# Performance work log

Measured on AMD Instinct MI355X. Metric: run time of the kernel, lower is better.

The kernel has to match this reference:

```python
import jax, jax.numpy as jnp
import numpy as np

V, T, NS, NH, E, H = 4, 4, 100000, 12288, 100000, 64
NEG_SLOPE = 0.01  # nn.LeakyReLU default


def setup_inputs() -> dict:
    key = jax.random.key(0)
    k1, k2, k3, k4, k5 = jax.random.split(key, 5)
    x = jax.random.normal(k1, (V, T, NS), dtype=jnp.float32)          # per-var, per-t scalar node features
    src_idx = jax.random.randint(k2, (V, T, E), 0, NS, dtype=jnp.int32)
    dst_idx = jax.random.randint(k3, (V, T, E), 0, NH, dtype=jnp.int32)
    W = jax.random.normal(k4, (V, T, H), dtype=jnp.float32)            # GraphConv weight, in_feats=1 -> [1,H] per etype
    b = jax.random.normal(k5, (V, T, H), dtype=jnp.float32) * 0.02     # GraphConv bias per etype
    return {"x": x, "W": W, "b": b, "src_idx": src_idx, "dst_idx": dst_idx, "n_healpix": NH}


def reference(x, W, b, src_idx, dst_idx, n_healpix):
    # x: [V,T,NS]; W,b: [V,T,H]; src_idx,dst_idx: [V,T,E]
    x = jnp.nan_to_num(x, nan=0.0)

    def conv_scalar(x_v, src, dst):
        # x_v: [T,NS] (all timestep features for this var), src/dst: [E] for ONE edge type
        ones = jnp.ones(src.shape, x_v.dtype)
        deg_out = jax.ops.segment_sum(ones, src, num_segments=NS)       # out-degree of src nodes
        deg_in = jax.ops.segment_sum(ones, dst, num_segments=n_healpix)  # in-degree of dst nodes
        norm_src = jax.lax.rsqrt(jnp.maximum(deg_out, 1.0))
        norm_dst = jax.lax.rsqrt(jnp.maximum(deg_in, 1.0))
        msg = x_v[:, src] * norm_src[src]                                # [T,E] gather
        agg = jax.vmap(lambda m: jax.ops.segment_sum(m, dst, num_segments=n_healpix))(msg)  # [T,NH]
        return agg * norm_dst                                            # norm='both'

    # HeteroGraphConv bug-faithful: for each var, EVERY per-t' conv is applied to each x[:,t]
    # s[v, t', t, n] = normalized scatter of x[v,t] through edges of etype t'
    s = jax.vmap(lambda xv, sv, dv: jax.vmap(lambda se, de: conv_scalar(xv, se, de))(sv, dv))(
        x, src_idx, dst_idx)                                             # [V,T',T,NH]

    # in_feats=1: linear is outer product with W row; bias + LeakyReLU inside each conv, sum over etypes t'
    h = jax.nn.leaky_relu(s[..., None] * W[:, :, None, None, :] + b[:, :, None, None, :],
                          negative_slope=NEG_SLOPE)                      # [V,T',T,NH,H]
    out = h.sum(axis=1)                                                  # aggregate='sum' over edge types -> [V,T,NH,H]
    # final stacking: stack over t (dim=1) then over vars (dim=1) -> [NH, V, T, H]
    return jnp.transpose(out, (2, 0, 1, 3))
```

## Files before the change

### kernel.cpp

```cpp
#include <hip/hip_runtime.h>
#include <math.h>

#define V    4
#define T    4
#define NSRC 100000
#define NHX  12288
#define E    100000
#define H    64
#define VT   16

#define SL    16
#define SLE   (E/SL)
#define RCH   2
#define RBINS (NSRC/RCH)
#define RW    (RBINS/4)
#define HF    8
#define HE    (E/HF)
#define NW    (NSRC/4)
#define NCH   12
#define NPB   8

#define S1_TRANS  391
#define S1_CNT    (RCH*HF*VT)
#define S1_DHIST  (SL*VT)
#define S2_SCAN   (NCH*VT)
#define S2_NSFIN  391

typedef float vf4 __attribute__((ext_vector_type(4)));

__global__ void __launch_bounds__(1024)
s1_kernel(const float* __restrict__ x, const int* __restrict__ src,
          const int* __restrict__ dst, float4* __restrict__ x4,
          unsigned int* __restrict__ cnt_part, unsigned int* __restrict__ ph,
          unsigned int* __restrict__ cs) {
    __shared__ unsigned int lds[RW];
    const int b = blockIdx.x, tid = threadIdx.x;

    if (b < S1_TRANS) {
        const int g = b * 1024 + tid;
        if (g < V * NSRC) {
            const int v = g / NSRC, s = g - v * NSRC;
            const float* xr = x + (size_t)v * T * NSRC + s;
            float a0 = xr[0], a1 = xr[NSRC], a2 = xr[2 * NSRC], a3 = xr[3 * NSRC];
            float4 r;
            r.x = (a0 == a0) ? a0 : 0.0f;
            r.y = (a1 == a1) ? a1 : 0.0f;
            r.z = (a2 == a2) ? a2 : 0.0f;
            r.w = (a3 == a3) ? a3 : 0.0f;
            x4[g] = r;
        }
        return;
    }
    if (b < S1_TRANS + S1_CNT) {
        const int idx = b - S1_TRANS;
        const int rg = idx & 1;
        const int hf = (idx >> 1) & 7;
        const int vt = idx >> 4;
        const int lo = rg * RBINS;
        for (int i = tid; i < RW; i += 1024) lds[i] = 0u;
        __syncthreads();
        const int* s_row = src + vt * E + hf * HE;
        for (int e = tid; e < HE; e += 1024) {
            const unsigned r = (unsigned)(s_row[e] - lo);
            if (r < RBINS) atomicAdd(&lds[r >> 2], 1u << ((r & 3) * 8));
        }
        __syncthreads();
        unsigned int* outp = cnt_part + ((size_t)hf * VT + vt) * NW + rg * RW;
        for (int i = tid; i < RW; i += 1024) outp[i] = lds[i];
        return;
    }
    {
        const int idx = b - (S1_TRANS + S1_CNT);
        const int sl = idx & 15, vt = idx >> 4;
        for (int i = tid; i < NHX; i += 1024) lds[i] = 0u;
        __syncthreads();
        const int* d_row = dst + vt * E + sl * SLE;
        for (int e = tid; e < SLE; e += 1024)
            atomicAdd(&lds[d_row[e]], 1u);
        __syncthreads();
        unsigned int* outp = ph + ((size_t)vt * SL + sl) * NHX;
        for (int i = tid; i < NHX; i += 1024) outp[i] = lds[i];
        const int lane = tid & 63, wv = tid >> 6;
        if (wv < NCH) {
            unsigned int s = 0;
#pragma unroll
            for (int i = 0; i < 16; ++i) s += lds[wv * 1024 + i * 64 + lane];
#pragma unroll
            for (int off = 32; off > 0; off >>= 1)
                s += (unsigned int)__shfl_down((int)s, off, 64);
            if (lane == 0) cs[((size_t)vt * SL + sl) * NCH + wv] = s;
        }
    }
}

__global__ void __launch_bounds__(1024)
s2_kernel(const unsigned int* __restrict__ cnt_part,
          const unsigned int* __restrict__ ph,
          const unsigned int* __restrict__ cs,
          float4* __restrict__ ns4,
          unsigned int* __restrict__ start,
          unsigned int* __restrict__ colstart,
          unsigned int* __restrict__ degs) {
    const int b = blockIdx.x, tid = threadIdx.x;

    if (b < S2_SCAN) {
        const int vt = b & 15, ch = b >> 4;
        const int lane = tid & 63, wv = tid >> 6;
        const int d = ch * 1024 + tid;
        __shared__ unsigned int wsum[16];
        __shared__ unsigned int sbase;
        if (wv == 0) {
            unsigned int p = 0;
            if (lane < SL)
                for (int c = 0; c < ch; ++c)
                    p += cs[((size_t)vt * SL + lane) * NCH + c];
#pragma unroll
            for (int off = 8; off > 0; off >>= 1)
                p += (unsigned int)__shfl_down((int)p, off, 64);
            if (lane == 0) sbase = p;
        }
        unsigned int h[SL];
        unsigned int tot = 0;
#pragma unroll
        for (int s = 0; s < SL; ++s) {
            h[s] = ph[((size_t)vt * SL + s) * NHX + d];
            tot += h[s];
        }
        unsigned int incl = tot;
#pragma unroll
        for (int off = 1; off < 64; off <<= 1) {
            const unsigned int vup = (unsigned int)__shfl_up((int)incl, off, 64);
            if (lane >= off) incl += vup;
        }
        if (lane == 63) wsum[wv] = incl;
        __syncthreads();
        if (tid == 0) {
            unsigned int run = sbase;
#pragma unroll
            for (int w = 0; w < 16; ++w) { const unsigned int t2 = wsum[w]; wsum[w] = run; run += t2; }
        }
        __syncthreads();
        const unsigned int excl = wsum[wv] + (incl - tot);
        const size_t vd = (size_t)vt * NHX + d;
        colstart[vd] = excl;
        degs[vd]     = tot;
        unsigned int acc = excl;
#pragma unroll
        for (int s = 0; s < SL; ++s) {
            start[((size_t)vt * SL + s) * NHX + d] = acc;
            acc += h[s];
        }
        return;
    }
    {
        const int g = (b - S2_SCAN) * 1024 + tid;
        if (g >= VT * NW) return;
        unsigned c0 = 0, c1 = 0, c2 = 0, c3 = 0;
#pragma unroll
        for (int hf = 0; hf < HF; ++hf) {
            const unsigned w = cnt_part[(size_t)hf * VT * NW + g];
            c0 += w & 0xFFu; c1 += (w >> 8) & 0xFFu;
            c2 += (w >> 16) & 0xFFu; c3 += w >> 24;
        }
        float4 r;
        r.x = rsqrtf(fmaxf((float)c0, 1.0f));
        r.y = rsqrtf(fmaxf((float)c1, 1.0f));
        r.z = rsqrtf(fmaxf((float)c2, 1.0f));
        r.w = rsqrtf(fmaxf((float)c3, 1.0f));
        ns4[g] = r;
    }
}

__global__ void __launch_bounds__(1024)
s3_reorder(const int* __restrict__ src, const int* __restrict__ dst,
           const unsigned int* __restrict__ start, int* __restrict__ sorted) {
    const int b = blockIdx.x;
    const int k = b & 7, j = b >> 3;
    const int vt = 2 * k + (j & 1);
    const int sl = j >> 1;
    __shared__ unsigned int pos[NHX];
    const unsigned int* st = start + ((size_t)vt * SL + sl) * NHX;
    for (int i = threadIdx.x; i < NHX; i += 1024) pos[i] = st[i];
    __syncthreads();
    const int* s_row = src + vt * E + sl * SLE;
    const int* d_row = dst + vt * E + sl * SLE;
    int* outp = sorted + (size_t)vt * E;
    for (int e = threadIdx.x; e < SLE; e += 1024) {
        const int d = d_row[e];
        const int s = s_row[e];
        const unsigned int p = atomicAdd(&pos[d], 1u);
        outp[p] = s;
    }
}

__global__ void __launch_bounds__(256)
s4_accum(const float4* __restrict__ x4, const int* __restrict__ sorted,
         const float* __restrict__ ns,
         const unsigned int* __restrict__ colstart,
         const unsigned int* __restrict__ degs,
         float4* __restrict__ sval) {
    const int b = blockIdx.x;
    const int k = b & 7, j = b >> 3;
    const int vt = 2 * k + (j & 1);
    const int chunk = j >> 1;
    const int d = chunk * 128 + (threadIdx.x >> 1);
    const int half = threadIdx.x & 1;
    const int v = vt >> 2;
    const size_t vd = (size_t)vt * NHX + d;
    const unsigned int base = colstart[vd];
    const unsigned int deg  = degs[vd];
    const int*    srt    = sorted + (size_t)vt * E;
    const float*  ns_row = ns + (size_t)vt * NSRC;
    const float4* x_row  = x4 + (size_t)v * NSRC;
    float4 acc = make_float4(0.f, 0.f, 0.f, 0.f);
    for (unsigned int i = half; i < deg; i += 2) {
        const int s = srt[base + i];
        const float4 xa = x_row[s];
        const float  na = ns_row[s];
        acc.x += xa.x * na; acc.y += xa.y * na;
        acc.z += xa.z * na; acc.w += xa.w * na;
    }
    acc.x += __shfl_xor(acc.x, 1, 64);
    acc.y += __shfl_xor(acc.y, 1, 64);
    acc.z += __shfl_xor(acc.z, 1, 64);
    acc.w += __shfl_xor(acc.w, 1, 64);
    if (half == 0) {
        const float nd = rsqrtf(fmaxf((float)deg, 1.0f));
        acc.x *= nd; acc.y *= nd; acc.z *= nd; acc.w *= nd;
        sval[vd] = acc;
    }
}

__global__ void __launch_bounds__(256)
s5_epilogue(const float4* __restrict__ sval, const float* __restrict__ Wm,
            const float* __restrict__ bm, float* __restrict__ out) {
    const int n0  = blockIdx.x * NPB;
    const int tid = threadIdx.x;
    __shared__ float sW[VT * H];
    __shared__ float sb[VT * H];
    __shared__ float sv[VT][T][NPB];

    for (int i = tid; i < VT * H; i += 256) { sW[i] = Wm[i]; sb[i] = bm[i]; }
    if (tid < VT * NPB) {
        const int vt = tid >> 3, n = tid & 7;
        const float4 r = sval[(size_t)vt * NHX + n0 + n];
        sv[vt][0][n] = r.x; sv[vt][1][n] = r.y;
        sv[vt][2][n] = r.z; sv[vt][3][n] = r.w;
    }
    __syncthreads();

    const int v  = tid >> 6;
    const int t  = (tid >> 4) & 3;
    const int hb = (tid & 15) * 4;
    float4 Wr[4], Br[4];
#pragma unroll
    for (int tp = 0; tp < 4; ++tp) {
        const int wi = (v * 4 + tp) * H + hb;
        Wr[tp] = *(const float4*)&sW[wi];
        Br[tp] = *(const float4*)&sb[wi];
    }
#pragma unroll
    for (int n = 0; n < NPB; ++n) {
        float4 o = make_float4(0.f, 0.f, 0.f, 0.f);
#pragma unroll
        for (int tp = 0; tp < 4; ++tp) {
            const float s = sv[v * 4 + tp][t][n];
            float a;
            a = fmaf(s, Wr[tp].x, Br[tp].x); o.x += (a > 0.f) ? a : 0.01f * a;
            a = fmaf(s, Wr[tp].y, Br[tp].y); o.y += (a > 0.f) ? a : 0.01f * a;
            a = fmaf(s, Wr[tp].z, Br[tp].z); o.z += (a > 0.f) ? a : 0.01f * a;
            a = fmaf(s, Wr[tp].w, Br[tp].w); o.w += (a > 0.f) ? a : 0.01f * a;
        }
        vf4* dstp = (vf4*)(out + (size_t)(n0 + n) * (V * T * H)) + tid;
        __builtin_nontemporal_store(*(vf4*)&o, dstp);
    }
}

extern "C" void kernel_launch(void* const* d_in, const int* in_sizes, int n_in,
                              void* d_out, int out_size, void* d_ws, size_t ws_size,
                              hipStream_t stream) {
    const float* x   = (const float*)d_in[0];
    const float* Wm  = (const float*)d_in[1];
    const float* bm  = (const float*)d_in[2];
    const int*   src = (const int*)d_in[3];
    const int*   dst = (const int*)d_in[4];
    float* out = (float*)d_out;

    char* ws = (char*)d_ws;
    size_t off = 0;
    float4* x4 = (float4*)(ws + off);                   off += (size_t)V * NSRC * 16;
    float4* sval = (float4*)(ws + off);                 off += (size_t)VT * NHX * 16;
    float4* ns4 = (float4*)(ws + off);                  off += (size_t)VT * NSRC * 4;
    unsigned int* ph = (unsigned int*)(ws + off);       off += (size_t)VT * SL * NHX * 4;
    unsigned int* start = (unsigned int*)(ws + off);    off += (size_t)VT * SL * NHX * 4;
    unsigned int* colstart = (unsigned int*)(ws + off); off += (size_t)VT * NHX * 4;
    unsigned int* degs = (unsigned int*)(ws + off);     off += (size_t)VT * NHX * 4;
    unsigned int* cs = (unsigned int*)(ws + off);       off += (size_t)VT * SL * NCH * 4;
    unsigned int* cnt_part = (unsigned int*)(ws + off); off += (size_t)HF * VT * NW * 4;
    int* sorted = (int*)(ws + off);                     off += (size_t)VT * E * 4;
    float* ns = (float*)ns4;

    s1_kernel<<<S1_TRANS + S1_CNT + S1_DHIST, 1024, 0, stream>>>(
        x, src, dst, x4, cnt_part, ph, cs);
    s2_kernel<<<S2_SCAN + S2_NSFIN, 1024, 0, stream>>>(
        cnt_part, ph, cs, ns4, start, colstart, degs);
    s3_reorder<<<SL * VT, 1024, 0, stream>>>(src, dst, start, sorted);
    s4_accum<<<1536, 256, 0, stream>>>(x4, sorted, ns, colstart, degs, sval);
    s5_epilogue<<<NHX / NPB, 256, 0, stream>>>(sval, Wm, bm, out);
}
```

Before: 145.3 us.

## Fuse scan into reorder kernel and store partial dst histograms as 16-bit

Merges the separate scan stage into the reorder kernel. Each reorder block recomputes the column prefix scan for its (vt, slice) from the partial histograms and builds its own start positions in LDS, so the start array and one kernel launch go away. The partial histograms are stored as uint16 to halve their traffic. In exchange, every one of the 16 slice blocks per vt repeats the full 12-chunk scan, adding redundant reads and many block-wide barriers before the scatter phase.

```diff
diff --git a/kernel.cpp b/kernel.cpp
--- a/kernel.cpp
+++ b/kernel.cpp
@@ -23,15 +23,15 @@
 #define S1_TRANS  391
 #define S1_CNT    (RCH*HF*VT)
 #define S1_DHIST  (SL*VT)
-#define S2_SCAN   (NCH*VT)
-#define S2_NSFIN  391
+#define S3_REORD  (SL*VT)
+#define S3_NSFIN  391
 
 typedef float vf4 __attribute__((ext_vector_type(4)));
 
 __global__ void __launch_bounds__(1024)
 s1_kernel(const float* __restrict__ x, const int* __restrict__ src,
           const int* __restrict__ dst, float4* __restrict__ x4,
-          unsigned int* __restrict__ cnt_part, unsigned int* __restrict__ ph,
+          unsigned int* __restrict__ cnt_part, unsigned short* __restrict__ ph16,
           unsigned int* __restrict__ cs) {
     __shared__ unsigned int lds[RW];
     const int b = blockIdx.x, tid = threadIdx.x;
@@ -78,8 +78,9 @@
         for (int e = tid; e < SLE; e += 1024)
             atomicAdd(&lds[d_row[e]], 1u);
         __syncthreads();
-        unsigned int* outp = ph + ((size_t)vt * SL + sl) * NHX;
-        for (int i = tid; i < NHX; i += 1024) outp[i] = lds[i];
+        unsigned short* outp = ph16 + ((size_t)vt * SL + sl) * NHX;
+        for (int i = tid; i < NHX; i += 1024)
+            outp[i] = (unsigned short)lds[i];
         const int lane = tid & 63, wv = tid >> 6;
         if (wv < NCH) {
             unsigned int s = 0;
@@ -94,66 +95,18 @@
 }
 
 __global__ void __launch_bounds__(1024)
-s2_kernel(const unsigned int* __restrict__ cnt_part,
-          const unsigned int* __restrict__ ph,
+s3_kernel(const int* __restrict__ src, const int* __restrict__ dst,
+          const unsigned short* __restrict__ ph16,
           const unsigned int* __restrict__ cs,
-          float4* __restrict__ ns4,
-          unsigned int* __restrict__ start,
+          const unsigned int* __restrict__ cnt_part,
+          int* __restrict__ sorted,
           unsigned int* __restrict__ colstart,
-          unsigned int* __restrict__ degs) {
+          unsigned int* __restrict__ degs,
+          float4* __restrict__ ns4) {
     const int b = blockIdx.x, tid = threadIdx.x;
 
-    if (b < S2_SCAN) {
-        const int vt = b & 15, ch = b >> 4;
-        const int lane = tid & 63, wv = tid >> 6;
-        const int d = ch * 1024 + tid;
-        __shared__ unsigned int wsum[16];
-        __shared__ unsigned int sbase;
-        if (wv == 0) {
-            unsigned int p = 0;
-            if (lane < SL)
-                for (int c = 0; c < ch; ++c)
-                    p += cs[((size_t)vt * SL + lane) * NCH + c];
-#pragma unroll
-            for (int off = 8; off > 0; off >>= 1)
-                p += (unsigned int)__shfl_down((int)p, off, 64);
-            if (lane == 0) sbase = p;
-        }
-        unsigned int h[SL];
-        unsigned int tot = 0;
-#pragma unroll
-        for (int s = 0; s < SL; ++s) {
-            h[s] = ph[((size_t)vt * SL + s) * NHX + d];
-            tot += h[s];
-        }
-        unsigned int incl = tot;
-#pragma unroll
-        for (int off = 1; off < 64; off <<= 1) {
-            const unsigned int vup = (unsigned int)__shfl_up((int)incl, off, 64);
-            if (lane >= off) incl += vup;
-        }
-        if (lane == 63) wsum[wv] = incl;
-        __syncthreads();
-        if (tid == 0) {
-            unsigned int run = sbase;
-#pragma unroll
-            for (int w = 0; w < 16; ++w) { const unsigned int t2 = wsum[w]; wsum[w] = run; run += t2; }
-        }
-        __syncthreads();
-        const unsigned int excl = wsum[wv] + (incl - tot);
-        const size_t vd = (size_t)vt * NHX + d;
-        colstart[vd] = excl;
-        degs[vd]     = tot;
-        unsigned int acc = excl;
-#pragma unroll
-        for (int s = 0; s < SL; ++s) {
-            start[((size_t)vt * SL + s) * NHX + d] = acc;
-            acc += h[s];
-        }
-        return;
-    }
-    {
-        const int g = (b - S2_SCAN) * 1024 + tid;
+    if (b >= S3_REORD) {
+        const int g = (b - S3_REORD) * 1024 + tid;
         if (g >= VT * NW) return;
         unsigned c0 = 0, c1 = 0, c2 = 0, c3 = 0;
 #pragma unroll
@@ -168,24 +121,70 @@
         r.z = rsqrtf(fmaxf((float)c2, 1.0f));
         r.w = rsqrtf(fmaxf((float)c3, 1.0f));
         ns4[g] = r;
-    }
-}
-
-__global__ void __launch_bounds__(1024)
-s3_reorder(const int* __restrict__ src, const int* __restrict__ dst,
-           const unsigned int* __restrict__ start, int* __restrict__ sorted) {
-    const int b = blockIdx.x;
+        return;
+    }
+
     const int k = b & 7, j = b >> 3;
     const int vt = 2 * k + (j & 1);
     const int sl = j >> 1;
+    const int lane = tid & 63, wv = tid >> 6;
+
     __shared__ unsigned int pos[NHX];
-    const unsigned int* st = start + ((size_t)vt * SL + sl) * NHX;
-    for (int i = threadIdx.x; i < NHX; i += 1024) pos[i] = st[i];
+    __shared__ unsigned int wsum[16];
+    __shared__ unsigned int cum[NCH];
+
+    if (tid < NCH) {
+        unsigned int s = 0;
+#pragma unroll
+        for (int q = 0; q < SL; ++q)
+            s += cs[((size_t)vt * SL + q) * NCH + tid];
+        cum[tid] = s;
+    }
     __syncthreads();
+    if (tid == 0) {
+        unsigned int run = 0;
+#pragma unroll
+        for (int c = 0; c < NCH; ++c) { const unsigned int t2 = cum[c]; cum[c] = run; run += t2; }
+    }
+    __syncthreads();
+
+    for (int ch = 0; ch < NCH; ++ch) {
+        const int d = ch * 1024 + tid;
+        unsigned int tot = 0, pre = 0;
+#pragma unroll
+        for (int q = 0; q < SL; ++q) {
+            const unsigned int hv = ph16[((size_t)vt * SL + q) * NHX + d];
+            tot += hv;
+            if (q < sl) pre += hv;
+        }
+        unsigned int incl = tot;
+#pragma unroll
+        for (int off = 1; off < 64; off <<= 1) {
+            const unsigned int vup = (unsigned int)__shfl_up((int)incl, off, 64);
+            if (lane >= off) incl += vup;
+        }
+        if (lane == 63) wsum[wv] = incl;
+        __syncthreads();
+        if (tid == 0) {
+            unsigned int run = cum[ch];
+#pragma unroll
+            for (int w = 0; w < 16; ++w) { const unsigned int t2 = wsum[w]; wsum[w] = run; run += t2; }
+        }
+        __syncthreads();
+        const unsigned int excl = wsum[wv] + (incl - tot);
+        pos[d] = excl + pre;
+        if (sl == 0) {
+            const size_t vd = (size_t)vt * NHX + d;
+            colstart[vd] = excl;
+            degs[vd]     = tot;
+        }
+        __syncthreads();
+    }
+
     const int* s_row = src + vt * E + sl * SLE;
     const int* d_row = dst + vt * E + sl * SLE;
     int* outp = sorted + (size_t)vt * E;
-    for (int e = threadIdx.x; e < SLE; e += 1024) {
+    for (int e = tid; e < SLE; e += 1024) {
         const int d = d_row[e];
         const int s = s_row[e];
         const unsigned int p = atomicAdd(&pos[d], 1u);
@@ -291,8 +290,7 @@
     float4* x4 = (float4*)(ws + off);                   off += (size_t)V * NSRC * 16;
     float4* sval = (float4*)(ws + off);                 off += (size_t)VT * NHX * 16;
     float4* ns4 = (float4*)(ws + off);                  off += (size_t)VT * NSRC * 4;
-    unsigned int* ph = (unsigned int*)(ws + off);       off += (size_t)VT * SL * NHX * 4;
-    unsigned int* start = (unsigned int*)(ws + off);    off += (size_t)VT * SL * NHX * 4;
+    unsigned short* ph16 = (unsigned short*)(ws + off); off += (size_t)VT * SL * NHX * 2;
     unsigned int* colstart = (unsigned int*)(ws + off); off += (size_t)VT * NHX * 4;
     unsigned int* degs = (unsigned int*)(ws + off);     off += (size_t)VT * NHX * 4;
     unsigned int* cs = (unsigned int*)(ws + off);       off += (size_t)VT * SL * NCH * 4;
@@ -301,10 +299,9 @@
     float* ns = (float*)ns4;
 
     s1_kernel<<<S1_TRANS + S1_CNT + S1_DHIST, 1024, 0, stream>>>(
-        x, src, dst, x4, cnt_part, ph, cs);
-    s2_kernel<<<S2_SCAN + S2_NSFIN, 1024, 0, stream>>>(
-        cnt_part, ph, cs, ns4, start, colstart, degs);
-    s3_reorder<<<SL * VT, 1024, 0, stream>>>(src, dst, start, sorted);
+        x, src, dst, x4, cnt_part, ph16, cs);
+    s3_kernel<<<S3_REORD + S3_NSFIN, 1024, 0, stream>>>(
+        src, dst, ph16, cs, cnt_part, sorted, colstart, degs, ns4);
     s4_accum<<<1536, 256, 0, stream>>>(x4, sorted, ns, colstart, degs, sval);
     s5_epilogue<<<NHX / NPB, 256, 0, stream>>>(sval, Wm, bm, out);
 }
```

Result: slower. 153.2 us (+5.4%).

## Pre-scale gathered features in reorder and fuse accumulation into epilogue

Applied to the files above, without the earlier changes.

The reorder pass now gathers x4 and the source normalization and writes pre-scaled float4 values in dst-sorted order, instead of writing source indices. The accumulation step then becomes a contiguous segmented sum, done directly inside the epilogue kernel, which removes the separate s4 launch and the sval round trip. The per-slice dst histogram is also stored as 16-bit counts to halve that traffic. In exchange, the sorted buffer grows from 4 to 16 bytes per edge, and the reduction runs with only 256 threads per 8-node block inside the epilogue, so that work may be less parallel.

```diff
diff --git a/kernel.cpp b/kernel.cpp
--- a/kernel.cpp
+++ b/kernel.cpp
@@ -31,7 +31,7 @@
 __global__ void __launch_bounds__(1024)
 s1_kernel(const float* __restrict__ x, const int* __restrict__ src,
           const int* __restrict__ dst, float4* __restrict__ x4,
-          unsigned int* __restrict__ cnt_part, unsigned int* __restrict__ ph,
+          unsigned int* __restrict__ cnt_part, unsigned short* __restrict__ ph16,
           unsigned int* __restrict__ cs) {
     __shared__ unsigned int lds[RW];
     const int b = blockIdx.x, tid = threadIdx.x;
@@ -78,8 +78,9 @@
         for (int e = tid; e < SLE; e += 1024)
             atomicAdd(&lds[d_row[e]], 1u);
         __syncthreads();
-        unsigned int* outp = ph + ((size_t)vt * SL + sl) * NHX;
-        for (int i = tid; i < NHX; i += 1024) outp[i] = lds[i];
+        unsigned short* outp = ph16 + ((size_t)vt * SL + sl) * NHX;
+        for (int i = tid; i < NHX; i += 1024)
+            outp[i] = (unsigned short)lds[i];
         const int lane = tid & 63, wv = tid >> 6;
         if (wv < NCH) {
             unsigned int s = 0;
@@ -95,7 +96,7 @@
 
 __global__ void __launch_bounds__(1024)
 s2_kernel(const unsigned int* __restrict__ cnt_part,
-          const unsigned int* __restrict__ ph,
+          const unsigned short* __restrict__ ph16,
           const unsigned int* __restrict__ cs,
           float4* __restrict__ ns4,
           unsigned int* __restrict__ start,
@@ -123,7 +124,7 @@
         unsigned int tot = 0;
 #pragma unroll
         for (int s = 0; s < SL; ++s) {
-            h[s] = ph[((size_t)vt * SL + s) * NHX + d];
+            h[s] = ph16[((size_t)vt * SL + s) * NHX + d];
             tot += h[s];
         }
         unsigned int incl = tot;
@@ -173,67 +174,42 @@
 
 __global__ void __launch_bounds__(1024)
 s3_reorder(const int* __restrict__ src, const int* __restrict__ dst,
-           const unsigned int* __restrict__ start, int* __restrict__ sorted) {
+           const unsigned int* __restrict__ start,
+           const float4* __restrict__ x4, const float* __restrict__ ns,
+           float4* __restrict__ xs) {
     const int b = blockIdx.x;
     const int k = b & 7, j = b >> 3;
     const int vt = 2 * k + (j & 1);
     const int sl = j >> 1;
+    const int v = vt >> 2;
     __shared__ unsigned int pos[NHX];
     const unsigned int* st = start + ((size_t)vt * SL + sl) * NHX;
     for (int i = threadIdx.x; i < NHX; i += 1024) pos[i] = st[i];
     __syncthreads();
     const int* s_row = src + vt * E + sl * SLE;
     const int* d_row = dst + vt * E + sl * SLE;
-    int* outp = sorted + (size_t)vt * E;
+    const float*  ns_row = ns + (size_t)vt * NSRC;
+    const float4* x_row  = x4 + (size_t)v * NSRC;
+    float4* xs_row = xs + (size_t)vt * E;
     for (int e = threadIdx.x; e < SLE; e += 1024) {
         const int d = d_row[e];
         const int s = s_row[e];
         const unsigned int p = atomicAdd(&pos[d], 1u);
-        outp[p] = s;
+        const float4 xv = x_row[s];
+        const float  nv = ns_row[s];
+        float4 r;
+        r.x = xv.x * nv; r.y = xv.y * nv;
+        r.z = xv.z * nv; r.w = xv.w * nv;
+        xs_row[p] = r;
     }
 }
 
 __global__ void __launch_bounds__(256)
-s4_accum(const float4* __restrict__ x4, const int* __restrict__ sorted,
-         const float* __restrict__ ns,
-         const unsigned int* __restrict__ colstart,
-         const unsigned int* __restrict__ degs,
-         float4* __restrict__ sval) {
-    const int b = blockIdx.x;
-    const int k = b & 7, j = b >> 3;
-    const int vt = 2 * k + (j & 1);
-    const int chunk = j >> 1;
-    const int d = chunk * 128 + (threadIdx.x >> 1);
-    const int half = threadIdx.x & 1;
-    const int v = vt >> 2;
-    const size_t vd = (size_t)vt * NHX + d;
-    const unsigned int base = colstart[vd];
-    const unsigned int deg  = degs[vd];
-    const int*    srt    = sorted + (size_t)vt * E;
-    const float*  ns_row = ns + (size_t)vt * NSRC;
-    const float4* x_row  = x4 + (size_t)v * NSRC;
-    float4 acc = make_float4(0.f, 0.f, 0.f, 0.f);
-    for (unsigned int i = half; i < deg; i += 2) {
-        const int s = srt[base + i];
-        const float4 xa = x_row[s];
-        const float  na = ns_row[s];
-        acc.x += xa.x * na; acc.y += xa.y * na;
-        acc.z += xa.z * na; acc.w += xa.w * na;
-    }
-    acc.x += __shfl_xor(acc.x, 1, 64);
-    acc.y += __shfl_xor(acc.y, 1, 64);
-    acc.z += __shfl_xor(acc.z, 1, 64);
-    acc.w += __shfl_xor(acc.w, 1, 64);
-    if (half == 0) {
-        const float nd = rsqrtf(fmaxf((float)deg, 1.0f));
-        acc.x *= nd; acc.y *= nd; acc.z *= nd; acc.w *= nd;
-        sval[vd] = acc;
-    }
-}
-
-__global__ void __launch_bounds__(256)
-s5_epilogue(const float4* __restrict__ sval, const float* __restrict__ Wm,
-            const float* __restrict__ bm, float* __restrict__ out) {
+s45_kernel(const float4* __restrict__ xs,
+           const unsigned int* __restrict__ colstart,
+           const unsigned int* __restrict__ degs,
+           const float* __restrict__ Wm, const float* __restrict__ bm,
+           float* __restrict__ out) {
     const int n0  = blockIdx.x * NPB;
     const int tid = threadIdx.x;
     __shared__ float sW[VT * H];
@@ -241,11 +217,29 @@
     __shared__ float sv[VT][T][NPB];
 
     for (int i = tid; i < VT * H; i += 256) { sW[i] = Wm[i]; sb[i] = bm[i]; }
-    if (tid < VT * NPB) {
-        const int vt = tid >> 3, n = tid & 7;
-        const float4 r = sval[(size_t)vt * NHX + n0 + n];
-        sv[vt][0][n] = r.x; sv[vt][1][n] = r.y;
-        sv[vt][2][n] = r.z; sv[vt][3][n] = r.w;
+
+    {
+        const int seg  = tid >> 1;
+        const int half = tid & 1;
+        const int vt = seg >> 3, n = seg & 7;
+        const size_t vd = (size_t)vt * NHX + (n0 + n);
+        const unsigned int base = colstart[vd];
+        const unsigned int deg  = degs[vd];
+        const float4* xrow = xs + (size_t)vt * E;
+        float4 acc = make_float4(0.f, 0.f, 0.f, 0.f);
+        for (unsigned int i = half; i < deg; i += 2) {
+            const float4 a = xrow[base + i];
+            acc.x += a.x; acc.y += a.y; acc.z += a.z; acc.w += a.w;
+        }
+        acc.x += __shfl_xor(acc.x, 1, 64);
+        acc.y += __shfl_xor(acc.y, 1, 64);
+        acc.z += __shfl_xor(acc.z, 1, 64);
+        acc.w += __shfl_xor(acc.w, 1, 64);
+        if (half == 0) {
+            const float nd = rsqrtf(fmaxf((float)deg, 1.0f));
+            sv[vt][0][n] = acc.x * nd; sv[vt][1][n] = acc.y * nd;
+            sv[vt][2][n] = acc.z * nd; sv[vt][3][n] = acc.w * nd;
+        }
     }
     __syncthreads();
 
@@ -289,22 +283,20 @@
     char* ws = (char*)d_ws;
     size_t off = 0;
     float4* x4 = (float4*)(ws + off);                   off += (size_t)V * NSRC * 16;
-    float4* sval = (float4*)(ws + off);                 off += (size_t)VT * NHX * 16;
     float4* ns4 = (float4*)(ws + off);                  off += (size_t)VT * NSRC * 4;
-    unsigned int* ph = (unsigned int*)(ws + off);       off += (size_t)VT * SL * NHX * 4;
+    unsigned short* ph16 = (unsigned short*)(ws + off); off += (size_t)VT * SL * NHX * 2;
     unsigned int* start = (unsigned int*)(ws + off);    off += (size_t)VT * SL * NHX * 4;
     unsigned int* colstart = (unsigned int*)(ws + off); off += (size_t)VT * NHX * 4;
     unsigned int* degs = (unsigned int*)(ws + off);     off += (size_t)VT * NHX * 4;
     unsigned int* cs = (unsigned int*)(ws + off);       off += (size_t)VT * SL * NCH * 4;
     unsigned int* cnt_part = (unsigned int*)(ws + off); off += (size_t)HF * VT * NW * 4;
-    int* sorted = (int*)(ws + off);                     off += (size_t)VT * E * 4;
+    float4* xs = (float4*)(ws + off);                   off += (size_t)VT * E * 16;
     float* ns = (float*)ns4;
 
     s1_kernel<<<S1_TRANS + S1_CNT + S1_DHIST, 1024, 0, stream>>>(
-        x, src, dst, x4, cnt_part, ph, cs);
+        x, src, dst, x4, cnt_part, ph16, cs);
     s2_kernel<<<S2_SCAN + S2_NSFIN, 1024, 0, stream>>>(
-        cnt_part, ph, cs, ns4, start, colstart, degs);
-    s3_reorder<<<SL * VT, 1024, 0, stream>>>(src, dst, start, sorted);
-    s4_accum<<<1536, 256, 0, stream>>>(x4, sorted, ns, colstart, degs, sval);
-    s5_epilogue<<<NHX / NPB, 256, 0, stream>>>(sval, Wm, bm, out);
-}
+        cnt_part, ph16, cs, ns4, start, colstart, degs);
+    s3_reorder<<<SL * VT, 1024, 0, stream>>>(src, dst, start, x4, ns, xs);
+    s45_kernel<<<NHX / NPB, 256, 0, stream>>>(xs, colstart, degs, Wm, bm, out);
+}
```

After: 155.5 us. 7.0% more time.
